# Performance work log

Hardware: AMD Instinct MI355X
Metric: run time of the kernel (lower is better)

The kernel has to match this reference:

```python
import jax, jax.numpy as jnp
import numpy as np
from jax import lax


def _spectral_topk_filter(X, k):
    # X: complex (B, Freq, F). Keep top-k magnitude freqs per (batch, feature).
    Xt = jnp.transpose(X, (0, 2, 1))  # (B, F, Freq)
    mag = jnp.abs(Xt)
    _, idx = lax.top_k(mag, k)  # (B, F, k)
    vals = jnp.take_along_axis(Xt, idx, axis=-1)
    B, F, _ = Xt.shape
    bi = jnp.arange(B)[:, None, None]
    fi = jnp.arange(F)[None, :, None]
    filt = jnp.zeros_like(Xt).at[bi, fi, idx].set(vals)
    return jnp.transpose(filt, (0, 2, 1))  # (B, Freq, F)


def _hamming_periodic(W):
    # matches torch.hamming_window(W) default (periodic=True)
    n = jnp.arange(W, dtype=jnp.float32)
    return 0.54 - 0.46 * jnp.cos(2.0 * jnp.pi * n / W)


def setup_inputs() -> dict:
    key = jax.random.key(0)
    x = jax.random.normal(key, (32, 4096, 128), dtype=jnp.float32)
    return {"x": x, "window_size": 25, "k": 16}


def reference(x, window_size, k):
    B, T, F = x.shape
    W = window_size
    half = W // 2

    # spectral filter: rfft -> keep top-k freqs -> irfft
    X = jnp.fft.rfft(x, axis=1)
    Xf = _spectral_topk_filter(X, k)
    xf = jnp.fft.irfft(Xf, axis=1).astype(x.dtype)  # (B, T, F)

    # flip-padding as in the torch module
    left = xf[:, :half, :][:, ::-1, :]
    right = xf[:, -half:, :][:, ::-1, :]
    xp = jnp.concatenate([left, xf, right], axis=1)  # (B, T + 2*half, F)

    # sliding hamming-window average == depthwise 1D correlation (no kernel flip,
    # matching the elementwise multiply in the original loop)
    w = _hamming_periodic(W).astype(x.dtype)
    xr = jnp.transpose(xp, (0, 2, 1)).reshape(B * F, 1, -1)  # (B*F, 1, Tp)
    out = lax.conv_general_dilated(xr, w[None, None, :], (1,), 'VALID')  # (B*F, 1, T)
    out = out.reshape(B, F, T).transpose(0, 2, 1) / jnp.sum(w)
    return out
```

## Files before the change

### kernel.cpp

```cpp
#include <hip/hip_runtime.h>
#include <math.h>


#define NN     4096
#define LOGN   12
#define NT     256
#define EPT    16
#define KTOP   16
#define WSZ    25
#define HALFW  12
#define FDIM   128
#define BATCH  32
#define RECL   88
#define TT     128
#define TWO_PI 6.283185307179586f

__device__ __forceinline__ int swz(int a) { return a + (a >> 5); }

#define CMUL(r, i, wr_, wi_) { float _r = (r); (r) = _r * (wr_) - (i) * (wi_); (i) = _r * (wi_) + (i) * (wr_); }
#define MULNI(r, i)          { float _r = (r); (r) = (i); (i) = -_r; }

__device__ __forceinline__ void cs_phase(int ph, float& c, float& s)
{
    const float rev = (float)ph * (1.0f / (float)NN);
    s = __builtin_amdgcn_sinf(rev);
    c = __builtin_amdgcn_cosf(rev);
}

__device__ __forceinline__ void dft16(float (&zr)[16], float (&zi)[16])
{
    const float C1 = 0.92387953251128674f;
    const float S1 = 0.38268343236508978f;
    const float R2 = 0.70710678118654752f;
    float yr[16], yi[16];
    #pragma unroll
    for (int n2 = 0; n2 < 4; ++n2) {
        float ar = zr[n2],      ai = zi[n2];
        float br = zr[4 + n2],  bi = zi[4 + n2];
        float cr = zr[8 + n2],  ci = zi[8 + n2];
        float dr = zr[12 + n2], di = zi[12 + n2];
        float t0r = ar + cr, t0i = ai + ci;
        float t1r = ar - cr, t1i = ai - ci;
        float t2r = br + dr, t2i = bi + di;
        float t3r = br - dr, t3i = bi - di;
        yr[n2]      = t0r + t2r;  yi[n2]      = t0i + t2i;
        yr[4 + n2]  = t1r + t3i;  yi[4 + n2]  = t1i - t3r;
        yr[8 + n2]  = t0r - t2r;  yi[8 + n2]  = t0i - t2i;
        yr[12 + n2] = t1r - t3i;  yi[12 + n2] = t1i + t3r;
    }
    CMUL(yr[5],  yi[5],  C1, -S1);
    CMUL(yr[6],  yi[6],  R2, -R2);
    CMUL(yr[7],  yi[7],  S1, -C1);
    CMUL(yr[9],  yi[9],  R2, -R2);
    MULNI(yr[10], yi[10]);
    CMUL(yr[11], yi[11], -R2, -R2);
    CMUL(yr[13], yi[13], S1, -C1);
    CMUL(yr[14], yi[14], -R2, -R2);
    CMUL(yr[15], yi[15], -C1, S1);
    #pragma unroll
    for (int k1 = 0; k1 < 4; ++k1) {
        float ar = yr[k1 * 4 + 0], ai = yi[k1 * 4 + 0];
        float br = yr[k1 * 4 + 1], bi = yi[k1 * 4 + 1];
        float cr = yr[k1 * 4 + 2], ci = yi[k1 * 4 + 2];
        float dr = yr[k1 * 4 + 3], di = yi[k1 * 4 + 3];
        float t0r = ar + cr, t0i = ai + ci;
        float t1r = ar - cr, t1i = ai - ci;
        float t2r = br + dr, t2i = bi + di;
        float t3r = br - dr, t3i = bi - di;
        zr[k1]      = t0r + t2r;  zi[k1]      = t0i + t2i;
        zr[4 + k1]  = t1r + t3i;  zi[4 + k1]  = t1i - t3r;
        zr[8 + k1]  = t0r - t2r;  zi[8 + k1]  = t0i - t2i;
        zr[12 + k1] = t1r - t3i;  zi[12 + k1] = t1i + t3r;
    }
}

__global__ __launch_bounds__(NT, 4)
void spectral_fft_kernel(const float* __restrict__ x, float* __restrict__ ws)
{
    __shared__ float s_re[NN + (NN >> 5)];
    __shared__ float s_im[NN + (NN >> 5)];
    __shared__ float s_w[WSZ];
    __shared__ float s_wsum;
    __shared__ float s_rv[8];
    __shared__ int   s_rk[8];
    __shared__ int   s_kf[KTOP];
    __shared__ float s_kr[KTOP];
    __shared__ float s_ki[KTOP];
    __shared__ float s_vr[KTOP];
    __shared__ float s_vi[KTOP];
    __shared__ float s_cd2[KTOP];
    __shared__ float s_edge[2 * HALFW];
    __shared__ float s_dl[2 * HALFW];

    const int tid = threadIdx.x;

    const int p  = blockIdx.x;
    const int wg = ((p & 7) << 9) + (p >> 3);
    const int b  = wg >> 7;
    const int f  = wg & (FDIM - 1);
    const float* xc = x + (size_t)b * NN * FDIM + f;

    if (tid < WSZ)
        s_w[tid] = 0.54f - 0.46f * cosf(TWO_PI * (float)tid / (float)WSZ);

    float zr[16], zi[16];
    #pragma unroll
    for (int r = 0; r < 16; ++r) { zr[r] = xc[(tid + (r << 8)) * FDIM]; zi[r] = 0.0f; }

    dft16(zr, zi);

    if (tid == 0) {
        float a = 0.0f;
        for (int i = 0; i < WSZ; ++i) a += s_w[i];
        s_wsum = a;
    }

    {
        float sn, cs;
        sincosf(-TWO_PI * (float)tid / (float)NN, &sn, &cs);
        float dr = cs, di = sn;
        float wr = dr, wi = di;
        #pragma unroll
        for (int u = 1; u < 16; ++u) {
            CMUL(zr[u], zi[u], wr, wi);
            float nr = wr * dr - wi * di; wi = wr * di + wi * dr; wr = nr;
        }
        #pragma unroll
        for (int u = 0; u < 16; ++u) {
            int a = swz(tid + (u << 8));
            s_re[a] = zr[u]; s_im[a] = zi[u];
        }
    }
    __syncthreads();

    {
        const int pp = tid & 15;
        const int b0 = ((tid >> 4) << 8) + pp;
        #pragma unroll
        for (int r = 0; r < 16; ++r) {
            int a = swz(b0 + (r << 4));
            zr[r] = s_re[a]; zi[r] = s_im[a];
        }
        dft16(zr, zi);
        float sn, cs;
        sincosf(-TWO_PI * (float)(pp << 4) / (float)NN, &sn, &cs);
        float dr = cs, di = sn;
        float wr = dr, wi = di;
        #pragma unroll
        for (int u = 1; u < 16; ++u) {
            CMUL(zr[u], zi[u], wr, wi);
            float nr = wr * dr - wi * di; wi = wr * di + wi * dr; wr = nr;
        }
        #pragma unroll
        for (int u = 0; u < 16; ++u) {
            int a = swz(b0 + (u << 4));
            s_re[a] = zr[u]; s_im[a] = zi[u];
        }
    }
    __syncthreads();

    {
        #pragma unroll
        for (int r = 0; r < 16; ++r) {
            int a = swz((tid << 4) + r);
            zr[r] = s_re[a]; zi[r] = s_im[a];
        }
        dft16(zr, zi);
    }

    const int fbase = ((tid & 15) << 4) | (tid >> 4);
    float mg[9];
    float lmax = -1.0f; int lk = 0x7fffffff;
    #pragma unroll
    for (int u = 0; u < 9; ++u) {
        float v = zr[u] * zr[u] + zi[u] * zi[u];
        if (u == 8 && fbase != 0) v = -1.0f;
        mg[u] = v;
        if (v > lmax) { lmax = v; lk = (u << 8) + fbase; }
    }

    for (int r = 0; r < KTOP; ++r) {
        float bv = lmax; int bk = lk;
        #pragma unroll
        for (int off = 32; off > 0; off >>= 1) {
            float ov = __shfl_down(bv, off);
            int   ok = __shfl_down(bk, off);
            if (ov > bv || (ov == bv && ok < bk)) { bv = ov; bk = ok; }
        }
        const int buf = (r & 1) << 2;
        if ((tid & 63) == 0) { s_rv[buf + (tid >> 6)] = bv; s_rk[buf + (tid >> 6)] = bk; }
        __syncthreads();
        bv = s_rv[buf]; bk = s_rk[buf];
        #pragma unroll
        for (int w2 = 1; w2 < 4; ++w2) {
            float ov = s_rv[buf + w2]; int ok = s_rk[buf + w2];
            if (ov > bv || (ov == bv && ok < bk)) { bv = ov; bk = ok; }
        }
        if (lmax == bv && lk == bk) {
            const int uw = bk >> 8;
            s_kf[r] = bk;
            #pragma unroll
            for (int u2 = 0; u2 < 9; ++u2) {
                if (u2 == uw) { s_kr[r] = zr[u2]; s_ki[r] = zi[u2]; mg[u2] = -1.0f; }
            }
            lmax = -1.0f; lk = 0x7fffffff;
            #pragma unroll
            for (int u2 = 0; u2 < 9; ++u2) {
                float v = mg[u2];
                if (v > lmax) { lmax = v; lk = (u2 << 8) + fbase; }
            }
        }
    }
    __syncthreads();

    if (tid < 2 * HALFW) {
        const int te = (tid < HALFW) ? tid : (NN - 2 * HALFW + tid);
        float a = 0.0f;
        for (int r = 0; r < KTOP; ++r) {
            const int fj = s_kf[r];
            float vr = s_kr[r], vi = s_ki[r];
            if (fj == 0 || fj == NN / 2) { vi = 0.0f; }
            else { vr *= 2.0f; vi *= 2.0f; }
            float c, s;
            cs_phase((fj * te) & (NN - 1), c, s);
            a += vr * c - vi * s;
        }
        s_edge[tid] = a * (1.0f / (float)NN);
    }
    if (tid >= 64 && tid < 64 + KTOP) {
        const int r = tid - 64;
        const int fj = s_kf[r];
        float vr = s_kr[r], vi = s_ki[r];
        float sc;
        if (fj == 0 || fj == NN / 2) { vi = 0.0f; sc = 1.0f; }
        else                         { sc = 2.0f; }
        float cr, ci, dc, ds;
        cs_phase((-HALFW * fj) & (NN - 1), cr, ci);
        cs_phase(fj, dc, ds);
        float hr = 0.0f, hi = 0.0f;
        for (int i = 0; i < WSZ; ++i) {
            const float wv = s_w[i];
            hr += wv * cr; hi += wv * ci;
            float nc = cr * dc - ci * ds;
            ci = ci * dc + cr * ds;
            cr = nc;
        }
        const float scale = sc / ((float)NN * s_wsum);
        s_vr[r]  = (vr * hr - vi * hi) * scale;
        s_vi[r]  = (vr * hi + vi * hr) * scale;
        s_cd2[r] = dc + dc;
    }
    __syncthreads();

    if (tid == 0) {
        const float rinv = 1.0f / s_wsum;
        for (int t = 0; t < HALFW; ++t) {
            float d = 0.0f;
            for (int i = 0; t + i < HALFW; ++i)
                d += s_w[i] * (s_edge[HALFW - 1 - t - i] - s_edge[HALFW + t + i]);
            s_dl[t] = d * rinv;
        }
        for (int j = 0; j < HALFW; ++j) {
            float d = 0.0f;
            for (int i = 2 * HALFW - j; i < WSZ; ++i)
                d += s_w[i] * (s_edge[4 * HALFW - 1 - j - i] - s_edge[j + i - 2 * HALFW]);
            s_dl[HALFW + j] = d * rinv;
        }
    }
    __syncthreads();

    if (tid < RECL) {
        float v;
        if      (tid < 16) v = s_vr[tid];
        else if (tid < 32) v = s_vi[tid - 16];
        else if (tid < 48) v = s_cd2[tid - 32];
        else if (tid < 64) v = (float)s_kf[tid - 48];
        else               v = s_dl[tid - 64];
        ws[(size_t)wg * RECL + tid] = v;
    }
}

__global__ __launch_bounds__(NT, 4)
void spectral_recon_kernel(const float* __restrict__ ws, float* __restrict__ out)
{
    __shared__ float s_c[FDIM * 65];

    const int tid = threadIdx.x;
    const int tb  = blockIdx.x * TT;
    const int b   = blockIdx.y;
    const int chB = b * FDIM;

    #pragma unroll
    for (int k = 0; k < (FDIM * 64) / NT; ++k) {
        int idx = tid + (k << 8);
        int ch  = idx >> 6;
        int j   = idx & 63;
        s_c[ch * 65 + j] = ws[(size_t)(chB + ch) * RECL + j];
    }
    __syncthreads();

    const int m  = tid & 31;
    const int tq = tid >> 5;
    const int t0 = tb + tq * 16;

    float acc[4][16];
    #pragma unroll
    for (int c = 0; c < 4; ++c)
        #pragma unroll
        for (int i = 0; i < 16; ++i) acc[c][i] = 0.0f;

    for (int r = 0; r < KTOP; ++r) {
        #pragma unroll
        for (int c = 0; c < 4; ++c) {
            const float* rec = &s_c[(c * 32 + m) * 65];
            const float vr  = rec[r];
            const float vi  = rec[16 + r];
            const float cd2 = rec[32 + r];
            const int   fj  = (int)rec[48 + r];
            const int   p0  = (fj * t0) & (NN - 1);
            float c0, s0, cm, sm;
            cs_phase(p0, c0, s0);
            cs_phase((p0 - fj) & (NN - 1), cm, sm);
            float g1 = vr * c0 - vi * s0;
            float g0 = vr * cm - vi * sm;
            #pragma unroll
            for (int i = 0; i < 16; ++i) {
                acc[c][i] += g1;
                const float gn = __builtin_fmaf(cd2, g1, -g0);
                g0 = g1; g1 = gn;
            }
        }
    }

    #pragma unroll
    for (int c = 0; c < 4; ++c) {
        const int ch = c * 32 + m;
        if (tb == 0 && tq == 0) {
            #pragma unroll
            for (int i = 0; i < HALFW; ++i)
                acc[c][i] += ws[(size_t)(chB + ch) * RECL + 64 + i];
        }
        if (tb == NN - TT && tq == 7) {
            #pragma unroll
            for (int i = 4; i < 16; ++i)
                acc[c][i] += ws[(size_t)(chB + ch) * RECL + 76 + (i - 4)];
        }
        const size_t obase = ((size_t)b * NN + t0) * FDIM + ch;
        #pragma unroll
        for (int i = 0; i < 16; ++i)
            out[obase + (size_t)i * FDIM] = acc[c][i];
    }
}

__global__ __launch_bounds__(NT, 3)
void spectral_filter_fallback(const float* __restrict__ x, float* __restrict__ out)
{
    __shared__ float s_re[NN + (NN >> 5)];
    __shared__ float s_im[NN];
    __shared__ float s_tw[NN];
    __shared__ float s_w[WSZ];
    __shared__ float s_wsum;
    __shared__ float s_rv[NT / 64];
    __shared__ int   s_ri[NT / 64];
    __shared__ int   s_kf[KTOP];
    __shared__ float s_kr[KTOP];
    __shared__ float s_ki[KTOP];

    const int tid = threadIdx.x;
    const int c   = blockIdx.x;
    const int b   = c >> 7;
    const int f   = c & (FDIM - 1);
    const size_t base = (size_t)b * NN * FDIM + f;

    if (tid < WSZ)
        s_w[tid] = 0.54f - 0.46f * cosf(TWO_PI * (float)tid / (float)WSZ);

    for (int i = tid; i < NN / 2; i += NT) {
        float sn, cs;
        sincosf(-TWO_PI * (float)i / (float)NN, &sn, &cs);
        s_tw[i]          = cs;
        s_tw[i + NN / 2] = sn;
    }

    #pragma unroll
    for (int i = 0; i < EPT; ++i) {
        int j = tid + i * NT;
        int t = (int)(__brev((unsigned)j) >> (32 - LOGN));
        s_re[j] = x[base + (size_t)t * FDIM];
        s_im[j] = 0.0f;
    }
    __syncthreads();

    if (tid == 0) {
        float a = 0.0f;
        for (int i = 0; i < WSZ; ++i) a += s_w[i];
        s_wsum = a;
    }

    for (int s = 1; s <= LOGN; ++s) {
        const int half = 1 << (s - 1);
        const int tsh  = LOGN - s;
        #pragma unroll
        for (int i = 0; i < EPT / 2; ++i) {
            int j  = tid + i * NT;
            int p  = j & (half - 1);
            int i0 = ((j >> (s - 1)) << s) + p;
            int i1 = i0 + half;
            int q  = p << tsh;
            float wr = s_tw[q], wi = s_tw[q + NN / 2];
            float ar = s_re[i0], ai = s_im[i0];
            float br = s_re[i1], bi = s_im[i1];
            float tr = br * wr - bi * wi;
            float ti = br * wi + bi * wr;
            s_re[i0] = ar + tr;  s_im[i0] = ai + ti;
            s_re[i1] = ar - tr;  s_im[i1] = ai - ti;
        }
        __syncthreads();
    }

    for (int i = tid; i < NN / 2 + 1; i += NT) {
        float rr = s_re[i], ii = s_im[i];
        s_tw[i] = rr * rr + ii * ii;
    }
    __syncthreads();

    for (int r = 0; r < KTOP; ++r) {
        float best = -1.0f; int bidx = 0x7fffffff;
        for (int i = tid; i < NN / 2 + 1; i += NT) {
            float v = s_tw[i];
            if (v > best) { best = v; bidx = i; }
        }
        #pragma unroll
        for (int off = 32; off > 0; off >>= 1) {
            float ov = __shfl_down(best, off);
            int   oi = __shfl_down(bidx, off);
            if (ov > best || (ov == best && oi < bidx)) { best = ov; bidx = oi; }
        }
        const int wid = tid >> 6;
        if ((tid & 63) == 0) { s_rv[wid] = best; s_ri[wid] = bidx; }
        __syncthreads();
        if (tid == 0) {
            float bv = s_rv[0]; int bx = s_ri[0];
            #pragma unroll
            for (int w2 = 1; w2 < NT / 64; ++w2) {
                float ov = s_rv[w2]; int oi = s_ri[w2];
                if (ov > bv || (ov == bv && oi < bx)) { bv = ov; bx = oi; }
            }
            s_kf[r] = bx;
            s_kr[r] = s_re[bx];
            s_ki[r] = s_im[bx];
            s_tw[bx] = -1.0f;
        }
        __syncthreads();
    }

    const int t0 = tid * EPT;
    float xf[EPT];
    #pragma unroll
    for (int i = 0; i < EPT; ++i) xf[i] = 0.0f;

    for (int r = 0; r < KTOP; ++r) {
        const int fj = s_kf[r];
        float vr = s_kr[r], vi = s_ki[r];
        float sc = 2.0f;
        if (fj == 0 || fj == NN / 2) { sc = 1.0f; vi = 0.0f; }
        vr *= sc; vi *= sc;
        const int ph0 = (fj * t0) & (NN - 1);
        float c0, s0, dc, ds;
        sincosf((float)ph0 * (TWO_PI / (float)NN), &s0, &c0);
        sincosf((float)fj  * (TWO_PI / (float)NN), &ds, &dc);
        float cr = c0, ci = s0;
        #pragma unroll
        for (int i = 0; i < EPT; ++i) {
            xf[i] += vr * cr - vi * ci;
            float nc = cr * dc - ci * ds;
            ci = ci * dc + cr * ds;
            cr = nc;
        }
    }
    __syncthreads();

    #pragma unroll
    for (int i = 0; i < EPT; ++i)
        s_re[swz(t0 + i)] = xf[i] * (1.0f / (float)NN);
    __syncthreads();

    float win[EPT + WSZ - 1];
    #pragma unroll
    for (int i = 0; i < EPT + WSZ - 1; ++i) {
        int a = t0 + i - HALFW;
        if (a < 0)        a = -1 - a;
        else if (a >= NN) a = 2 * NN - 1 - a;
        win[i] = s_re[swz(a)];
    }

    const float rinv = 1.0f / s_wsum;
    float acc[EPT];
    #pragma unroll
    for (int t = 0; t < EPT; ++t) acc[t] = 0.0f;
    #pragma unroll
    for (int i = 0; i < WSZ; ++i) {
        const float wv = s_w[i];
        #pragma unroll
        for (int t = 0; t < EPT; ++t) acc[t] += win[t + i] * wv;
    }
    #pragma unroll
    for (int t = 0; t < EPT; ++t)
        out[base + (size_t)(t0 + t) * FDIM] = acc[t] * rinv;
}

extern "C" void kernel_launch(void* const* d_in, const int* in_sizes, int n_in,
                              void* d_out, int out_size, void* d_ws, size_t ws_size,
                              hipStream_t stream)
{
    const float* x = (const float*)d_in[0];
    float* out = (float*)d_out;
    const size_t need = (size_t)BATCH * FDIM * RECL * sizeof(float);
    if (ws_size >= need) {
        float* ws = (float*)d_ws;
        spectral_fft_kernel<<<dim3(BATCH * FDIM), NT, 0, stream>>>(x, ws);
        spectral_recon_kernel<<<dim3(NN / TT, BATCH), NT, 0, stream>>>(ws, out);
    } else {
        spectral_filter_fallback<<<dim3(BATCH * FDIM), NT, 0, stream>>>(x, out);
    }
}
```

Before: 249.1 us.

## Halve FFT shared memory, use per-wave top-k candidates, shrink reconstruct accumulators

The FFT kernel now transposes its real and imaginary parts through one shared buffer in two passes, which halves LDS use and allows raising launch bounds to 6 blocks per SM. Top-k selection now runs independently in each wave with xor shuffles to produce 16 candidates per wave, then a single wave merges them. This removes the block-wide barrier from each of the 16 rounds. The reconstruct kernel loops over channels with a 16-element accumulator instead of 64, cutting register pressure at the cost of more barriers and transposes in the FFT.

```diff
diff --git a/kernel.cpp b/kernel.cpp
--- a/kernel.cpp
+++ b/kernel.cpp
@@ -74,15 +74,16 @@
     }
 }
 
-__global__ __launch_bounds__(NT, 4)
+__global__ __launch_bounds__(NT, 6)
 void spectral_fft_kernel(const float* __restrict__ x, float* __restrict__ ws)
 {
-    __shared__ float s_re[NN + (NN >> 5)];
-    __shared__ float s_im[NN + (NN >> 5)];
+    __shared__ float s_x[NN + (NN >> 5)];
     __shared__ float s_w[WSZ];
     __shared__ float s_wsum;
-    __shared__ float s_rv[8];
-    __shared__ int   s_rk[8];
+    __shared__ float s_cv[64];
+    __shared__ int   s_ck[64];
+    __shared__ float s_cr[64];
+    __shared__ float s_ci[64];
     __shared__ int   s_kf[KTOP];
     __shared__ float s_kr[KTOP];
     __shared__ float s_ki[KTOP];
@@ -115,6 +116,8 @@
         s_wsum = a;
     }
 
+    const int b0 = ((tid >> 4) << 8) + (tid & 15);
+
     {
         float sn, cs;
         sincosf(-TWO_PI * (float)tid / (float)NN, &sn, &cs);
@@ -125,23 +128,22 @@
             CMUL(zr[u], zi[u], wr, wi);
             float nr = wr * dr - wi * di; wi = wr * di + wi * dr; wr = nr;
         }
-        #pragma unroll
-        for (int u = 0; u < 16; ++u) {
-            int a = swz(tid + (u << 8));
-            s_re[a] = zr[u]; s_im[a] = zi[u];
-        }
-    }
-    __syncthreads();
-
+    }
+    #pragma unroll
+    for (int u = 0; u < 16; ++u) s_x[swz(tid + (u << 8))] = zr[u];
+    __syncthreads();
+    #pragma unroll
+    for (int r = 0; r < 16; ++r) zr[r] = s_x[swz(b0 + (r << 4))];
+    __syncthreads();
+    #pragma unroll
+    for (int u = 0; u < 16; ++u) s_x[swz(tid + (u << 8))] = zi[u];
+    __syncthreads();
+    #pragma unroll
+    for (int r = 0; r < 16; ++r) zi[r] = s_x[swz(b0 + (r << 4))];
+
+    dft16(zr, zi);
     {
         const int pp = tid & 15;
-        const int b0 = ((tid >> 4) << 8) + pp;
-        #pragma unroll
-        for (int r = 0; r < 16; ++r) {
-            int a = swz(b0 + (r << 4));
-            zr[r] = s_re[a]; zi[r] = s_im[a];
-        }
-        dft16(zr, zi);
         float sn, cs;
         sincosf(-TWO_PI * (float)(pp << 4) / (float)NN, &sn, &cs);
         float dr = cs, di = sn;
@@ -151,22 +153,21 @@
             CMUL(zr[u], zi[u], wr, wi);
             float nr = wr * dr - wi * di; wi = wr * di + wi * dr; wr = nr;
         }
-        #pragma unroll
-        for (int u = 0; u < 16; ++u) {
-            int a = swz(b0 + (u << 4));
-            s_re[a] = zr[u]; s_im[a] = zi[u];
-        }
-    }
-    __syncthreads();
-
-    {
-        #pragma unroll
-        for (int r = 0; r < 16; ++r) {
-            int a = swz((tid << 4) + r);
-            zr[r] = s_re[a]; zi[r] = s_im[a];
-        }
-        dft16(zr, zi);
-    }
+    }
+    __syncthreads();
+    #pragma unroll
+    for (int u = 0; u < 16; ++u) s_x[swz(b0 + (u << 4))] = zr[u];
+    __syncthreads();
+    #pragma unroll
+    for (int r = 0; r < 16; ++r) zr[r] = s_x[swz((tid << 4) + r)];
+    __syncthreads();
+    #pragma unroll
+    for (int u = 0; u < 16; ++u) s_x[swz(b0 + (u << 4))] = zi[u];
+    __syncthreads();
+    #pragma unroll
+    for (int r = 0; r < 16; ++r) zi[r] = s_x[swz((tid << 4) + r)];
+
+    dft16(zr, zi);
 
     const int fbase = ((tid & 15) << 4) | (tid >> 4);
     float mg[9];
@@ -179,35 +180,47 @@
         if (v > lmax) { lmax = v; lk = (u << 8) + fbase; }
     }
 
+    const int lane = tid & 63;
+    const int wid  = tid >> 6;
     for (int r = 0; r < KTOP; ++r) {
         float bv = lmax; int bk = lk;
         #pragma unroll
-        for (int off = 32; off > 0; off >>= 1) {
-            float ov = __shfl_down(bv, off);
-            int   ok = __shfl_down(bk, off);
-            if (ov > bv || (ov == bv && ok < bk)) { bv = ov; bk = ok; }
-        }
-        const int buf = (r & 1) << 2;
-        if ((tid & 63) == 0) { s_rv[buf + (tid >> 6)] = bv; s_rk[buf + (tid >> 6)] = bk; }
-        __syncthreads();
-        bv = s_rv[buf]; bk = s_rk[buf];
-        #pragma unroll
-        for (int w2 = 1; w2 < 4; ++w2) {
-            float ov = s_rv[buf + w2]; int ok = s_rk[buf + w2];
+        for (int off = 1; off < 64; off <<= 1) {
+            float ov = __shfl_xor(bv, off);
+            int   ok = __shfl_xor(bk, off);
             if (ov > bv || (ov == bv && ok < bk)) { bv = ov; bk = ok; }
         }
         if (lmax == bv && lk == bk) {
             const int uw = bk >> 8;
-            s_kf[r] = bk;
             #pragma unroll
             for (int u2 = 0; u2 < 9; ++u2) {
-                if (u2 == uw) { s_kr[r] = zr[u2]; s_ki[r] = zi[u2]; mg[u2] = -1.0f; }
+                if (u2 == uw) { s_cr[wid * 16 + r] = zr[u2]; s_ci[wid * 16 + r] = zi[u2]; mg[u2] = -1.0f; }
             }
             lmax = -1.0f; lk = 0x7fffffff;
             #pragma unroll
             for (int u2 = 0; u2 < 9; ++u2) {
                 float v = mg[u2];
                 if (v > lmax) { lmax = v; lk = (u2 << 8) + fbase; }
+            }
+        }
+        if (lane == r) { s_cv[wid * 16 + r] = bv; s_ck[wid * 16 + r] = bk; }
+    }
+    __syncthreads();
+
+    if (tid < 64) {
+        float cv = s_cv[tid]; int ck = s_ck[tid];
+        float cr = s_cr[tid], ci = s_ci[tid];
+        for (int r = 0; r < KTOP; ++r) {
+            float bv = cv; int bk = ck;
+            #pragma unroll
+            for (int off = 1; off < 64; off <<= 1) {
+                float ov = __shfl_xor(bv, off);
+                int   ok = __shfl_xor(bk, off);
+                if (ov > bv || (ov == bv && ok < bk)) { bv = ov; bk = ok; }
+            }
+            if (cv == bv && ck == bk) {
+                s_kf[r] = bk; s_kr[r] = cr; s_ki[r] = ci;
+                cv = -1.0f; ck = 0x7fffffff;
             }
         }
     }
@@ -303,16 +316,16 @@
     const int tq = tid >> 5;
     const int t0 = tb + tq * 16;
 
-    float acc[4][16];
-    #pragma unroll
-    for (int c = 0; c < 4; ++c)
-        #pragma unroll
-        for (int i = 0; i < 16; ++i) acc[c][i] = 0.0f;
-
-    for (int r = 0; r < KTOP; ++r) {
-        #pragma unroll
-        for (int c = 0; c < 4; ++c) {
-            const float* rec = &s_c[(c * 32 + m) * 65];
+    #pragma unroll 1
+    for (int c = 0; c < 4; ++c) {
+        const int ch = c * 32 + m;
+        const float* rec = &s_c[ch * 65];
+
+        float acc[16];
+        #pragma unroll
+        for (int i = 0; i < 16; ++i) acc[i] = 0.0f;
+
+        for (int r = 0; r < KTOP; ++r) {
             const float vr  = rec[r];
             const float vi  = rec[16 + r];
             const float cd2 = rec[32 + r];
@@ -325,30 +338,26 @@
             float g0 = vr * cm - vi * sm;
             #pragma unroll
             for (int i = 0; i < 16; ++i) {
-                acc[c][i] += g1;
+                acc[i] += g1;
                 const float gn = __builtin_fmaf(cd2, g1, -g0);
                 g0 = g1; g1 = gn;
             }
         }
-    }
-
-    #pragma unroll
-    for (int c = 0; c < 4; ++c) {
-        const int ch = c * 32 + m;
+
         if (tb == 0 && tq == 0) {
             #pragma unroll
             for (int i = 0; i < HALFW; ++i)
-                acc[c][i] += ws[(size_t)(chB + ch) * RECL + 64 + i];
+                acc[i] += ws[(size_t)(chB + ch) * RECL + 64 + i];
         }
         if (tb == NN - TT && tq == 7) {
             #pragma unroll
             for (int i = 4; i < 16; ++i)
-                acc[c][i] += ws[(size_t)(chB + ch) * RECL + 76 + (i - 4)];
+                acc[i] += ws[(size_t)(chB + ch) * RECL + 76 + (i - 4)];
         }
         const size_t obase = ((size_t)b * NN + t0) * FDIM + ch;
         #pragma unroll
         for (int i = 0; i < 16; ++i)
-            out[obase + (size_t)i * FDIM] = acc[c][i];
+            out[obase + (size_t)i * FDIM] = acc[i];
     }
 }
 
```

Result: faster. 227.4 us (-8.7%).
